# Kernel optimization log

Measured on AMD Instinct MI355X. Metric: run time of the kernel, lower is better.

Reference implementation:

```python
import math
import jax, jax.numpy as jnp
import numpy as np

NUM_HEADS = 16

def setup_inputs() -> dict:
    key = jax.random.key(0)
    k1, k2, k3, k4, k5 = jax.random.split(key, 5)
    B, S, D = 8, 4096, 1024
    x = jax.random.normal(k1, (B, S, D), dtype=jnp.float32)
    W_qkv = jax.random.normal(k2, (D, 3 * D), dtype=jnp.float32) * (1.0 / math.sqrt(D))
    b_qkv = jax.random.normal(k3, (3 * D,), dtype=jnp.float32) * 0.02
    W_out = jax.random.normal(k4, (D, D), dtype=jnp.float32) * (1.0 / math.sqrt(D))
    b_out = jax.random.normal(k5, (D,), dtype=jnp.float32) * 0.02
    return {"x": x, "W_qkv": W_qkv, "b_qkv": b_qkv, "W_out": W_out, "b_out": b_out}

def reference(x, W_qkv, b_qkv, W_out, b_out):
    B, S, D = x.shape
    H = NUM_HEADS
    hd = D // H
    scale = 1.0 / math.sqrt(hd)
    # QKV projection: (B,S,D) -> (B,S,3D), reshaped to (B,S,H,3*hd)
    qkv = (x @ W_qkv + b_qkv).reshape(B, S, H, 3 * hd)
    q, k, v = jnp.split(qkv, 3, axis=-1)  # each (B,S,H,hd)
    # Faithful to source: no head permute, so attention is across the H heads
    # at each (batch, seq) position. scores: (B,S,H,H)
    scores = jnp.einsum('bsqd,bskd->bsqk', q, k) * scale
    attn = jax.nn.softmax(scores, axis=-1)
    values = jnp.einsum('bsqk,bskd->bsqd', attn, v).reshape(B, S, D)
    return values @ W_out + b_out
```

## Files before the change

### kernel.cpp

```cpp
#include <hip/hip_runtime.h>
#include <hip/hip_bf16.h>

#define TOKENS   32768
#define DMODEL   1024
#define THREE_D  3072

using u16 = unsigned short;
typedef __attribute__((ext_vector_type(8))) short short8;
typedef __attribute__((ext_vector_type(4))) float f32x4;

__device__ __forceinline__ float bf2f(u16 u) {
  union { unsigned int i; float f; } v; v.i = ((unsigned int)u) << 16; return v.f;
}
__device__ __forceinline__ u16 f2bf(float f) {
  __hip_bfloat16 h = __float2bfloat16(f);
  return *reinterpret_cast<u16*>(&h);
}

__device__ __forceinline__ void gload_lds16(const u16* g, u16* l) {
  __builtin_amdgcn_global_load_lds((const __attribute__((address_space(1))) void*)g,
                                   (__attribute__((address_space(3))) void*)l,
                                   16, 0, 0);
}

__global__ __launch_bounds__(256) void convert_f32_bf16(const float* __restrict__ in,
                                                        u16* __restrict__ out, long n) {
  long i = ((long)blockIdx.x * 256 + threadIdx.x) * 4;
  if (i >= n) return;
  float4 v = *reinterpret_cast<const float4*>(in + i);
  ushort4 o;
  o.x = f2bf(v.x); o.y = f2bf(v.y); o.z = f2bf(v.z); o.w = f2bf(v.w);
  *reinterpret_cast<ushort4*>(out + i) = o;
}

__global__ __launch_bounds__(256) void transpose_convert(const float* __restrict__ in,
                                                         u16* __restrict__ out,
                                                         int R, int C) {
  __shared__ u16 tile[32][33];
  const int bc = blockIdx.x * 32;
  const int br = blockIdx.y * 32;
  const int tx = threadIdx.x & 31;
  const int ty = threadIdx.x >> 5;
  #pragma unroll
  for (int i = 0; i < 32; i += 8)
    tile[ty + i][tx] = f2bf(in[(long)(br + ty + i) * C + bc + tx]);
  __syncthreads();
  #pragma unroll
  for (int i = 0; i < 32; i += 8)
    out[(long)(bc + ty + i) * R + br + tx] = tile[tx][ty + i];
}

#define BM 128
#define BN 128
#define BK 32

template <bool OUT_F32>
__global__ __launch_bounds__(256) void gemm_bt_bias(
    const u16* __restrict__ A, const u16* __restrict__ BT,
    const float* __restrict__ bias, void* __restrict__ Cv,
    int M, int N, int K, long a_stride, int a_grp) {
  __shared__ alignas(16) u16 As[BM * BK];
  __shared__ alignas(16) u16 Bs[BN * BK];

  const int tiles_n = N / BN;
  const int bm = (blockIdx.x / tiles_n) * BM;
  const int bn = (blockIdx.x % tiles_n) * BN;
  const int tid  = threadIdx.x;
  const int wave = tid >> 6;
  const int lane = tid & 63;
  const int wm   = (wave & 1) * 64;
  const int wn   = (wave >> 1) * 64;
  const int lrow = lane & 15;
  const int kq   = (lane >> 4) * 8;

  const int srow = wave * 32 + (lane >> 2);
  const int scol = (lane & 3) * 8;
  u16* alds0 = As + (wave * 32) * BK;
  u16* alds1 = As + (wave * 32 + 16) * BK;
  u16* blds0 = Bs + (wave * 32) * BK;
  u16* blds1 = Bs + (wave * 32 + 16) * BK;

  f32x4 acc[4][4];
  #pragma unroll
  for (int i = 0; i < 4; i++)
    #pragma unroll
    for (int j = 0; j < 4; j++) acc[i][j] = (f32x4){0.f, 0.f, 0.f, 0.f};

  for (int k0 = 0; k0 < K; k0 += BK) {
    const int c = k0 + scol;
    const long aoff = (long)(c >> 6) * a_grp + (c & 63);
    __syncthreads();
    gload_lds16(A  + (long)(bm + srow)      * a_stride + aoff, alds0);
    gload_lds16(A  + (long)(bm + srow + 16) * a_stride + aoff, alds1);
    gload_lds16(BT + (long)(bn + srow)      * K + k0 + scol, blds0);
    gload_lds16(BT + (long)(bn + srow + 16) * K + k0 + scol, blds1);
    __syncthreads();

    short8 a[4], b[4];
    #pragma unroll
    for (int mi = 0; mi < 4; mi++)
      a[mi] = *reinterpret_cast<const short8*>(&As[(wm + mi * 16 + lrow) * BK + kq]);
    #pragma unroll
    for (int ni = 0; ni < 4; ni++)
      b[ni] = *reinterpret_cast<const short8*>(&Bs[(wn + ni * 16 + lrow) * BK + kq]);
    #pragma unroll
    for (int mi = 0; mi < 4; mi++)
      #pragma unroll
      for (int ni = 0; ni < 4; ni++)
        acc[mi][ni] = __builtin_amdgcn_mfma_f32_16x16x32_bf16(a[mi], b[ni], acc[mi][ni], 0, 0, 0);
  }

  #pragma unroll
  for (int ni = 0; ni < 4; ni++) {
    const int col = bn + wn + ni * 16 + lrow;
    const float bv = bias[col];
    #pragma unroll
    for (int mi = 0; mi < 4; mi++) {
      #pragma unroll
      for (int r = 0; r < 4; r++) {
        const int row = bm + wm + mi * 16 + (lane >> 4) * 4 + r;
        const float val = acc[mi][ni][r] + bv;
        if (OUT_F32)
          ((float*)Cv)[(long)row * N + col] = val;
        else
          ((u16*)Cv)[(long)row * N + col] = f2bf(val);
      }
    }
  }
}

__global__ __launch_bounds__(256) void attn_local(u16* __restrict__ qkv) {
  __shared__ float p_s[4][16][16];
  const int tid  = threadIdx.x;
  const int wave = tid >> 6;
  const int lane = tid & 63;
  const int t    = blockIdx.x * 4 + wave;
  u16* row = qkv + (long)t * THREE_D;
  const int lrow = lane & 15;
  const int quad = lane >> 4;
  const int kq   = quad * 8;

  short8 a0 = *reinterpret_cast<const short8*>(row + lrow * 192 + kq);
  short8 a1 = *reinterpret_cast<const short8*>(row + lrow * 192 + 32 + kq);
  short8 b0 = *reinterpret_cast<const short8*>(row + lrow * 192 + 64 + kq);
  short8 b1 = *reinterpret_cast<const short8*>(row + lrow * 192 + 96 + kq);
  f32x4 s = {0.f, 0.f, 0.f, 0.f};
  s = __builtin_amdgcn_mfma_f32_16x16x32_bf16(a0, b0, s, 0, 0, 0);
  s = __builtin_amdgcn_mfma_f32_16x16x32_bf16(a1, b1, s, 0, 0, 0);

  const float scale = 0.125f;
  float p[4];
  #pragma unroll
  for (int r = 0; r < 4; r++) {
    float x = s[r] * scale;
    float m = x;
    #pragma unroll
    for (int mask = 1; mask < 16; mask <<= 1) m = fmaxf(m, __shfl_xor(m, mask));
    float e = __expf(x - m);
    float l = e;
    #pragma unroll
    for (int mask = 1; mask < 16; mask <<= 1) l += __shfl_xor(l, mask);
    p[r] = e / l;
  }
  #pragma unroll
  for (int r = 0; r < 4; r++) p_s[wave][quad * 4 + r][lrow] = p[r];
  __syncthreads();

  float o[16];
  #pragma unroll
  for (int i = 0; i < 16; i++) o[i] = 0.f;
  #pragma unroll
  for (int j = 0; j < 16; j++) {
    float vj = bf2f(row[j * 192 + 128 + lane]);
    #pragma unroll
    for (int i = 0; i < 16; i++) o[i] += p_s[wave][i][j] * vj;
  }
  #pragma unroll
  for (int i = 0; i < 16; i++)
    row[i * 192 + lane] = f2bf(o[i]);
}

extern "C" void kernel_launch(void* const* d_in, const int* in_sizes, int n_in,
                              void* d_out, int out_size, void* d_ws, size_t ws_size,
                              hipStream_t stream) {
  const float* x     = (const float*)d_in[0];
  const float* W_qkv = (const float*)d_in[1];
  const float* b_qkv = (const float*)d_in[2];
  const float* W_out = (const float*)d_in[3];
  const float* b_out = (const float*)d_in[4];
  float* out = (float*)d_out;

  char* ws = (char*)d_ws;
  u16* qkv   = (u16*)ws;  ws += (size_t)TOKENS * THREE_D * 2;
  u16* x_bf  = (u16*)ws;  ws += (size_t)TOKENS * DMODEL * 2;
  u16* wqkvT = (u16*)ws;  ws += (size_t)THREE_D * DMODEL * 2;
  u16* woutT = (u16*)ws;

  dim3 tb(256);
  convert_f32_bf16<<<dim3((TOKENS * DMODEL) / 1024), tb, 0, stream>>>(
      x, x_bf, (long)TOKENS * DMODEL);
  transpose_convert<<<dim3(THREE_D / 32, DMODEL / 32), tb, 0, stream>>>(W_qkv, wqkvT, DMODEL, THREE_D);
  transpose_convert<<<dim3(DMODEL / 32, DMODEL / 32), tb, 0, stream>>>(W_out, woutT, DMODEL, DMODEL);
  gemm_bt_bias<false><<<dim3((TOKENS / BM) * (THREE_D / BN)), tb, 0, stream>>>(
      x_bf, wqkvT, b_qkv, qkv, TOKENS, THREE_D, DMODEL, (long)DMODEL, 64);
  attn_local<<<dim3(TOKENS / 4), tb, 0, stream>>>(qkv);
  gemm_bt_bias<true><<<dim3((TOKENS / BM) * (DMODEL / BN)), tb, 0, stream>>>(
      qkv, woutT, b_out, out, TOKENS, DMODEL, DMODEL, (long)THREE_D, 192);
}
```

Baseline: 652.6 us.

## Double GEMM K-tile to 64 and XOR-swizzle LDS layout to avoid bank conflicts

Measured after the change: 646.2 us. Within noise of the previous version (-1.0%).

```diff
diff --git a/kernel.cpp b/kernel.cpp
--- a/kernel.cpp
+++ b/kernel.cpp
@@ -52,7 +52,7 @@
 
 #define BM 128
 #define BN 128
-#define BK 32
+#define BK 64
 
 template <bool OUT_F32>
 __global__ __launch_bounds__(256) void gemm_bt_bias(
@@ -71,14 +71,11 @@
   const int wm   = (wave & 1) * 64;
   const int wn   = (wave >> 1) * 64;
   const int lrow = lane & 15;
-  const int kq   = (lane >> 4) * 8;
-
-  const int srow = wave * 32 + (lane >> 2);
-  const int scol = (lane & 3) * 8;
-  u16* alds0 = As + (wave * 32) * BK;
-  u16* alds1 = As + (wave * 32 + 16) * BK;
-  u16* blds0 = Bs + (wave * 32) * BK;
-  u16* blds1 = Bs + (wave * 32 + 16) * BK;
+  const int quad = lane >> 4;
+
+  const int sr     = lane >> 3;
+  const int schunk = (lane & 7) ^ sr;
+  const int scol   = schunk * 8;
 
   f32x4 acc[4][4];
   #pragma unroll
@@ -87,27 +84,34 @@
     for (int j = 0; j < 4; j++) acc[i][j] = (f32x4){0.f, 0.f, 0.f, 0.f};
 
   for (int k0 = 0; k0 < K; k0 += BK) {
-    const int c = k0 + scol;
-    const long aoff = (long)(c >> 6) * a_grp + (c & 63);
+    const long aoff = (long)(k0 >> 6) * a_grp + scol;
     __syncthreads();
-    gload_lds16(A  + (long)(bm + srow)      * a_stride + aoff, alds0);
-    gload_lds16(A  + (long)(bm + srow + 16) * a_stride + aoff, alds1);
-    gload_lds16(BT + (long)(bn + srow)      * K + k0 + scol, blds0);
-    gload_lds16(BT + (long)(bn + srow + 16) * K + k0 + scol, blds1);
+    #pragma unroll
+    for (int r = 0; r < 4; r++) {
+      const int row = wave * 32 + r * 8 + sr;
+      gload_lds16(A  + (long)(bm + row) * a_stride + aoff, As + (wave * 32 + r * 8) * BK);
+      gload_lds16(BT + (long)(bn + row) * K + k0 + scol,  Bs + (wave * 32 + r * 8) * BK);
+    }
     __syncthreads();
 
-    short8 a[4], b[4];
-    #pragma unroll
-    for (int mi = 0; mi < 4; mi++)
-      a[mi] = *reinterpret_cast<const short8*>(&As[(wm + mi * 16 + lrow) * BK + kq]);
-    #pragma unroll
-    for (int ni = 0; ni < 4; ni++)
-      b[ni] = *reinterpret_cast<const short8*>(&Bs[(wn + ni * 16 + lrow) * BK + kq]);
-    #pragma unroll
-    for (int mi = 0; mi < 4; mi++)
+    #pragma unroll
+    for (int kh = 0; kh < 2; kh++) {
+      const int xs = lrow & 7;
+      short8 a[4], b[4];
+      #pragma unroll
+      for (int mi = 0; mi < 4; mi++)
+        a[mi] = *reinterpret_cast<const short8*>(
+            &As[(wm + mi * 16 + lrow) * BK + (((kh * 4 + quad) ^ xs) * 8)]);
       #pragma unroll
       for (int ni = 0; ni < 4; ni++)
-        acc[mi][ni] = __builtin_amdgcn_mfma_f32_16x16x32_bf16(a[mi], b[ni], acc[mi][ni], 0, 0, 0);
+        b[ni] = *reinterpret_cast<const short8*>(
+            &Bs[(wn + ni * 16 + lrow) * BK + (((kh * 4 + quad) ^ xs) * 8)]);
+      #pragma unroll
+      for (int mi = 0; mi < 4; mi++)
+        #pragma unroll
+        for (int ni = 0; ni < 4; ni++)
+          acc[mi][ni] = __builtin_amdgcn_mfma_f32_16x16x32_bf16(a[mi], b[ni], acc[mi][ni], 0, 0, 0);
+    }
   }
 
   #pragma unroll
```
